# Performance work log

Measured on AMD Instinct MI355X. Metric: run time of the kernel, lower is better.

The kernel has to match this reference:

```python
import jax, jax.numpy as jnp
import numpy as np

B, S, D = 2, 2048, 2048
H = 16
HD = D // H
SCALE = 1.0 / (HD ** 0.5)


def setup_inputs() -> dict:
    key = jax.random.key(0)
    ks = jax.random.split(key, 9)
    std = 0.02
    return {
        "x": jax.random.normal(ks[0], (B, S, D), dtype=jnp.float32),
        "q_w": jax.random.normal(ks[1], (D, D), dtype=jnp.float32) * std,
        "q_b": jax.random.normal(ks[2], (D,), dtype=jnp.float32) * std,
        "k_w": jax.random.normal(ks[3], (D, D), dtype=jnp.float32) * std,
        "k_b": jax.random.normal(ks[4], (D,), dtype=jnp.float32) * std,
        "v_w": jax.random.normal(ks[5], (D, D), dtype=jnp.float32) * std,
        "v_b": jax.random.normal(ks[6], (D,), dtype=jnp.float32) * std,
        "o_w": jax.random.normal(ks[7], (D, D), dtype=jnp.float32) * std,
        "o_b": jax.random.normal(ks[8], (D,), dtype=jnp.float32) * std,
    }


def reference(x, q_w, q_b, k_w, k_b, v_w, v_b, o_w, o_b):
    # torch Linear: y = x @ W.T + b  (weights stored [out, in])
    b, s, _ = x.shape
    dtype = x.dtype
    q = (x @ q_w.T + q_b).reshape(b, s, H, HD).transpose(0, 2, 1, 3)  # [B,H,S,HD]
    k = (x @ k_w.T + k_b).reshape(b, s, H, HD).transpose(0, 2, 1, 3)
    v = (x @ v_w.T + v_b).reshape(b, s, H, HD).transpose(0, 2, 1, 3)
    scores = jnp.einsum("bhqd,bhkd->bhqk", q, k) * SCALE  # [B,H,S,S]
    # causal mask: positions k > q get -inf (via triu(diagonal=1))
    causal = jnp.triu(jnp.ones((s, s), dtype=bool), k=1)
    scores = jnp.where(causal[None, None], -jnp.inf, scores)
    attn = jax.nn.softmax(scores.astype(jnp.float32), axis=-1).astype(dtype)
    out = jnp.einsum("bhqk,bhkd->bhqd", attn, v)  # [B,H,S,HD]
    out = out.transpose(0, 2, 1, 3).reshape(b, s, H * HD)
    return out @ o_w.T + o_b
```

## Files before the change

kernel.cpp:

```cpp
#include <hip/hip_runtime.h>
#include <hip/hip_bf16.h>

#define S_LEN 2048
#define DMODEL 2048
#define NH 16
#define HDIM 128
#define SCALE_F 0.08838834764831845f

typedef __attribute__((ext_vector_type(8))) short bf16x8;
typedef __attribute__((ext_vector_type(4))) float f32x4;

__device__ __forceinline__ unsigned short f2bf(float f) {
  unsigned int u = __float_as_uint(f);
  u += 0x7FFFu + ((u >> 16) & 1u);
  return (unsigned short)(u >> 16);
}

__device__ __forceinline__ void gload16(const void* g, void* l) {
  __builtin_amdgcn_global_load_lds(
      (const __attribute__((address_space(1))) unsigned int*)g,
      (__attribute__((address_space(3))) unsigned int*)l, 16, 0, 0);
}

__global__ __launch_bounds__(256) void cvt_all(
    const float* __restrict__ x, const float* __restrict__ qw,
    const float* __restrict__ kw, const float* __restrict__ vw,
    const float* __restrict__ ow, unsigned short* __restrict__ xb,
    unsigned short* __restrict__ wqkv, unsigned short* __restrict__ wo) {
  int i = blockIdx.x * blockDim.x + threadIdx.x;
  const float* src;
  unsigned short* dst;
  int off;
  if (i < 2097152) {
    src = x; dst = xb; off = i;
  } else {
    const int j = i - 2097152;
    const int wsel = j >> 20;
    off = j & 1048575;
    src = (wsel == 0) ? qw : (wsel == 1) ? kw : (wsel == 2) ? vw : ow;
    dst = (wsel == 0) ? wqkv
        : (wsel == 1) ? (wqkv + 4194304)
        : (wsel == 2) ? (wqkv + 8388608)
                      : wo;
  }
  const float4 v = *(const float4*)(src + (size_t)off * 4);
  ushort4 o;
  o.x = f2bf(v.x); o.y = f2bf(v.y); o.z = f2bf(v.z); o.w = f2bf(v.w);
  *(ushort4*)(dst + (size_t)off * 4) = o;
}

__device__ __forceinline__ void gemm_core_128x256(
    const unsigned short* __restrict__ Ag, const unsigned short* __restrict__ Wg,
    int m0, int n0, char* lds, int t, f32x4 (&acc)[4][4]) {
  const int lane = t & 63, w = t >> 6;
  const int wr = w >> 2, wc = w & 3;

#pragma unroll
  for (int mi = 0; mi < 4; ++mi)
#pragma unroll
    for (int nj = 0; nj < 4; ++nj)
#pragma unroll
      for (int e = 0; e < 4; ++e) acc[mi][nj][e] = 0.f;

  const int fr = lane & 15;
  const int sw16 = (((lane >> 4) ^ ((lane >> 1) & 3)) << 4);
  const int aRowBase = (wr * 64 + fr) * 64;
  const int bRowBase = (wc * 64 + fr) * 64;

  const int cg8 = (((t & 3) ^ ((t >> 3) & 3)) * 8);
  const unsigned short* sAbase = Ag + (m0 + (t >> 2)) * DMODEL + cg8;
  const unsigned short* sBbase0 = Wg + (n0 + (t >> 2)) * DMODEL + cg8;
  const unsigned short* sBbase1 = sBbase0 + 128 * DMODEL;
  char* dstW = lds + w * 1024;

  auto stage3 = [&](int Tc, int h, int buf) {
    const int koff = Tc * 64 + h * 32;
    gload16(sAbase + koff, dstW + buf * 16384 + h * 8192);
    gload16(sBbase0 + koff, dstW + 49152 + buf * 32768 + h * 16384);
    gload16(sBbase1 + koff, dstW + 49152 + buf * 32768 + h * 16384 + 8192);
  };

  auto phase = [&](int h, int bufR, int doStage, int TS, int bufS, int vm) {
    const int rA = bufR * 16384 + h * 8192;
    const int rB = 49152 + bufR * 32768 + h * 16384;
    bf16x8 a[4], b[4];
#pragma unroll
    for (int mi = 0; mi < 4; ++mi)
      a[mi] = *(const bf16x8*)(lds + rA + aRowBase + mi * 1024 + sw16);
#pragma unroll
    for (int nj = 0; nj < 4; ++nj)
      b[nj] = *(const bf16x8*)(lds + rB + bRowBase + nj * 1024 + sw16);
    if (doStage) stage3(TS, h, bufS);
    if (vm == 6) asm volatile("s_waitcnt vmcnt(6)" ::: "memory");
    if (vm == 0) asm volatile("s_waitcnt vmcnt(0)" ::: "memory");
    __builtin_amdgcn_s_barrier();
    __builtin_amdgcn_s_setprio(1);
#pragma unroll
    for (int mi = 0; mi < 4; ++mi)
#pragma unroll
      for (int nj = 0; nj < 4; ++nj)
        acc[mi][nj] = __builtin_amdgcn_mfma_f32_16x16x32_bf16(
            a[mi], b[nj], acc[mi][nj], 0, 0, 0);
    __builtin_amdgcn_s_setprio(0);
    __builtin_amdgcn_s_barrier();
  };

  stage3(0, 0, 0);
  stage3(0, 1, 0);
  stage3(1, 0, 1);
  stage3(1, 1, 1);
  asm volatile("s_waitcnt vmcnt(6)" ::: "memory");
  __builtin_amdgcn_s_barrier();

#pragma unroll 1
  for (int k3 = 0; k3 < 10; ++k3) {
    const int T = k3 * 3;
    phase(0, 0, 1, T + 2, 2, -1);
    phase(1, 0, 1, T + 2, 2, 6);
    phase(0, 1, 1, T + 3, 0, -1);
    phase(1, 1, 1, T + 3, 0, 6);
    phase(0, 2, 1, T + 4, 1, -1);
    phase(1, 2, 1, T + 4, 1, 6);
  }
  phase(0, 0, 0, 0, 0, -1);
  phase(1, 0, 0, 0, 0, 0);
  phase(0, 1, 0, 0, 0, -1);
  phase(1, 1, 0, 0, 0, -1);
}

__global__ __launch_bounds__(512, 1) void gemm_qkv(
    const unsigned short* __restrict__ A, const unsigned short* __restrict__ W,
    const float* __restrict__ qbias, const float* __restrict__ kbias,
    const float* __restrict__ vbias,
    unsigned short* __restrict__ qo, unsigned short* __restrict__ ko,
    unsigned short* __restrict__ vto) {
  extern __shared__ char lds[];
  const int t = threadIdx.x;
  const int swz = ((int)blockIdx.x & 7) * 96 + ((int)blockIdx.x >> 3);
  const int m0 = (swz & 31) * 128;
  const int n0 = (swz >> 5) * 256;

  f32x4 acc[4][4];
  gemm_core_128x256(A, W, m0, n0, lds, t, acc);

  const int lane = t & 63, w = t >> 6;
  const int wr = w >> 2, wc = w & 3;
  const int b_ = m0 >> 11;
  const int proj = n0 >> 11;
  const int nn_base = (n0 & 2047) + wc * 64;
  const float* bias = (proj == 0) ? qbias : ((proj == 1) ? kbias : vbias);
#pragma unroll
  for (int nj = 0; nj < 4; ++nj) {
    const int nn = nn_base + nj * 16 + (lane & 15);
    const int h = nn >> 7, hd = nn & 127;
    const float bv = bias[nn];
#pragma unroll
    for (int mi = 0; mi < 4; ++mi) {
      const int mrow = m0 + wr * 64 + mi * 16 + (lane >> 4) * 4;
      const int s = mrow & 2047;
      if (proj == 2) {
        unsigned short* dst = vto + ((b_ * NH + h) * HDIM + hd) * S_LEN + s;
        ushort4 pk;
        pk.x = f2bf(acc[mi][nj][0] + bv);
        pk.y = f2bf(acc[mi][nj][1] + bv);
        pk.z = f2bf(acc[mi][nj][2] + bv);
        pk.w = f2bf(acc[mi][nj][3] + bv);
        *(ushort4*)dst = pk;
      } else {
        unsigned short* dst =
            ((proj == 0) ? qo : ko) + ((b_ * NH + h) * S_LEN + s) * HDIM + hd;
#pragma unroll
        for (int r = 0; r < 4; r++) dst[r * HDIM] = f2bf(acc[mi][nj][r] + bv);
      }
    }
  }
}

__global__ __launch_bounds__(512, 1) void gemm_out(
    const unsigned short* __restrict__ A, const unsigned short* __restrict__ W,
    const float* __restrict__ bias, float* __restrict__ out) {
  extern __shared__ char lds[];
  const int t = threadIdx.x;
  const int swz = ((int)blockIdx.x & 7) * 32 + ((int)blockIdx.x >> 3);
  const int m0 = (swz & 31) * 128;
  const int n0 = (swz >> 5) * 256;

  f32x4 acc[4][4];
  gemm_core_128x256(A, W, m0, n0, lds, t, acc);

  const int lane = t & 63, w = t >> 6;
  const int wr = w >> 2, wc = w & 3;
#pragma unroll
  for (int nj = 0; nj < 4; ++nj) {
    const int n = n0 + wc * 64 + nj * 16 + (lane & 15);
    const float bv = bias[n];
#pragma unroll
    for (int mi = 0; mi < 4; ++mi) {
      const int mrow = m0 + wr * 64 + mi * 16 + (lane >> 4) * 4;
      float* dst = out + (size_t)mrow * DMODEL + n;
#pragma unroll
      for (int r = 0; r < 4; r++) dst[r * DMODEL] = acc[mi][nj][r] + bv;
    }
  }
}

__global__ __launch_bounds__(256, 2) void attn_fwd(
    const unsigned short* __restrict__ Q,
    const unsigned short* __restrict__ K,
    const unsigned short* __restrict__ VT,
    unsigned short* __restrict__ ctx) {
  __shared__ unsigned short Ks[2][64 * 128];
  __shared__ unsigned short Vs[2][128 * 64];
  __shared__ unsigned short Ps[4][16 * 64];
  const int t = threadIdx.x, lane = t & 63, w = t >> 6;
  const int bh = blockIdx.y;
  const unsigned short* Qb = Q + bh * (S_LEN * HDIM);
  const unsigned short* Kb = K + bh * (S_LEN * HDIM);
  const unsigned short* Vb = VT + bh * (HDIM * S_LEN);
  const int b_ = bh >> 4, h = bh & 15;

  auto stageKV = [&](int buf, int kv0) {
#pragma unroll
    for (int u = 0; u < 4; ++u) {
      const int c = t + u * 256;
      const int row = c >> 4, cc = c & 15;
      gload16(Kb + (kv0 + row) * HDIM + ((cc ^ (row & 7)) * 8),
              (char*)Ks[buf] + u * 4096 + w * 1024);
    }
#pragma unroll
    for (int u = 0; u < 4; ++u) {
      const int c = t + u * 256;
      const int row = c >> 3, cc = c & 7;
      gload16(Vb + row * S_LEN + kv0 + ((cc ^ (row & 7)) * 8),
              (char*)Vs[buf] + u * 4096 + w * 1024);
    }
  };

#pragma unroll 1
  for (int pi = 0; pi < 2; ++pi) {
    const int qtile = pi ? (31 - blockIdx.x) : blockIdx.x;
    const int q0 = qtile * 64 + w * 16;

    bf16x8 qf[4];
    {
      const unsigned short* qrow =
          Qb + (q0 + (lane & 15)) * HDIM + (lane >> 4) * 8;
#pragma unroll
      for (int dk = 0; dk < 4; dk++) qf[dk] = *(const bf16x8*)(qrow + dk * 32);
    }

    float mrow[4], lrow[4];
    f32x4 oacc[8];
#pragma unroll
    for (int r = 0; r < 4; r++) { mrow[r] = -__builtin_inff(); lrow[r] = 0.f; }
#pragma unroll
    for (int d = 0; d < 8; d++)
#pragma unroll
      for (int e = 0; e < 4; e++) oacc[d][e] = 0.f;

    const int nt = qtile + 1;
    stageKV(0, 0);
    __syncthreads();
    int cur = 0;

#pragma unroll 1
    for (int kt = 0; kt < nt; ++kt) {
      if (kt + 1 < nt) stageKV(cur ^ 1, (kt + 1) * 64);

      const unsigned short* Kc = Ks[cur];
      const unsigned short* Vc = Vs[cur];
      const int kv0 = kt * 64;

      f32x4 sacc[4];
#pragma unroll
      for (int ck = 0; ck < 4; ck++)
#pragma unroll
        for (int e = 0; e < 4; e++) sacc[ck][e] = 0.f;
      __builtin_amdgcn_s_setprio(1);
#pragma unroll
      for (int ck = 0; ck < 4; ++ck) {
        const int krow = ck * 16 + (lane & 15);
#pragma unroll
        for (int dk = 0; dk < 4; ++dk) {
          const int chunk = dk * 4 + (lane >> 4);
          const bf16x8 kf = *(const bf16x8*)((const char*)Kc + krow * 256 +
                                             ((chunk ^ (krow & 7)) << 4));
          sacc[ck] = __builtin_amdgcn_mfma_f32_16x16x32_bf16(qf[dk], kf,
                                                             sacc[ck], 0, 0, 0);
        }
      }
      __builtin_amdgcn_s_setprio(0);
#pragma unroll
      for (int ck = 0; ck < 4; ck++)
#pragma unroll
        for (int r = 0; r < 4; r++) sacc[ck][r] *= SCALE_F;
      if (kt == qtile) {
#pragma unroll
        for (int ck = 0; ck < 4; ck++) {
          const int col = kv0 + ck * 16 + (lane & 15);
#pragma unroll
          for (int r = 0; r < 4; r++) {
            const int rowq = q0 + (lane >> 4) * 4 + r;
            if (col > rowq) sacc[ck][r] = -__builtin_inff();
          }
        }
      }
      float tmax[4];
#pragma unroll
      for (int r = 0; r < 4; r++)
        tmax[r] = fmaxf(fmaxf(sacc[0][r], sacc[1][r]),
                        fmaxf(sacc[2][r], sacc[3][r]));
#pragma unroll
      for (int off = 1; off < 16; off <<= 1)
#pragma unroll
        for (int r = 0; r < 4; r++)
          tmax[r] = fmaxf(tmax[r], __shfl_xor(tmax[r], off, 64));
      bool need = false;
#pragma unroll
      for (int r = 0; r < 4; r++) need |= (tmax[r] > mrow[r] + 8.f);
      if (__any(need)) {
#pragma unroll
        for (int r = 0; r < 4; r++) {
          const float mn = fmaxf(mrow[r], tmax[r]);
          const float corr = __expf(mrow[r] - mn);
          mrow[r] = mn;
          lrow[r] *= corr;
#pragma unroll
          for (int d = 0; d < 8; d++) oacc[d][r] *= corr;
        }
      }
      float rsum[4] = {0.f, 0.f, 0.f, 0.f};
#pragma unroll
      for (int ck = 0; ck < 4; ck++)
#pragma unroll
        for (int r = 0; r < 4; r++) {
          const float p = __expf(sacc[ck][r] - mrow[r]);
          rsum[r] += p;
          const int prow = (lane >> 4) * 4 + r;
          const int pcol = ck * 16 + (lane & 15);
          *(unsigned short*)((char*)Ps[w] +
                             ((prow * 128 + pcol * 2) ^ ((prow & 7) << 4))) =
              f2bf(p);
        }
#pragma unroll
      for (int off = 1; off < 16; off <<= 1)
#pragma unroll
        for (int r = 0; r < 4; r++) rsum[r] += __shfl_xor(rsum[r], off, 64);
#pragma unroll
      for (int r = 0; r < 4; r++) lrow[r] += rsum[r];

      bf16x8 pf[2];
      {
        const int prow = lane & 15;
#pragma unroll
        for (int kk = 0; kk < 2; kk++) {
          const int chunk = kk * 4 + (lane >> 4);
          pf[kk] = *(const bf16x8*)((const char*)Ps[w] + prow * 128 +
                                    ((chunk ^ (prow & 7)) << 4));
        }
      }
      __builtin_amdgcn_s_setprio(1);
#pragma unroll
      for (int d = 0; d < 8; ++d) {
        const int vrow = d * 16 + (lane & 15);
#pragma unroll
        for (int kk = 0; kk < 2; ++kk) {
          const int chunk = kk * 4 + (lane >> 4);
          const bf16x8 vf = *(const bf16x8*)((const char*)Vc + vrow * 128 +
                                             ((chunk ^ (vrow & 7)) << 4));
          oacc[d] = __builtin_amdgcn_mfma_f32_16x16x32_bf16(pf[kk], vf, oacc[d],
                                                            0, 0, 0);
        }
      }
      __builtin_amdgcn_s_setprio(0);

      __syncthreads();
      cur ^= 1;
    }

#pragma unroll
    for (int r = 0; r < 4; r++) {
      const float inv = 1.f / lrow[r];
      const int srow = q0 + (lane >> 4) * 4 + r;
      unsigned short* dst =
          ctx + (b_ * S_LEN + srow) * DMODEL + h * HDIM + (lane & 15);
#pragma unroll
      for (int d = 0; d < 8; d++) dst[d * 16] = f2bf(oacc[d][r] * inv);
    }
  }
}

extern "C" void kernel_launch(void* const* d_in, const int* in_sizes, int n_in,
                              void* d_out, int out_size, void* d_ws,
                              size_t ws_size, hipStream_t stream) {
  const float* x  = (const float*)d_in[0];
  const float* qw = (const float*)d_in[1];
  const float* qb = (const float*)d_in[2];
  const float* kw = (const float*)d_in[3];
  const float* kb = (const float*)d_in[4];
  const float* vw = (const float*)d_in[5];
  const float* vb = (const float*)d_in[6];
  const float* ow = (const float*)d_in[7];
  const float* ob = (const float*)d_in[8];
  float* out = (float*)d_out;

  unsigned short* xb   = (unsigned short*)d_ws;
  unsigned short* wqkv = xb + (size_t)8388608;
  unsigned short* wo   = wqkv + (size_t)12582912;
  unsigned short* qt_  = wo + (size_t)4194304;
  unsigned short* kt_  = qt_ + (size_t)8388608;
  unsigned short* vt_  = kt_ + (size_t)8388608;
  unsigned short* ctx  = vt_ + (size_t)8388608;

  cvt_all<<<24576, 256, 0, stream>>>(x, qw, kw, vw, ow, xb, wqkv, wo);

  gemm_qkv<<<768, 512, 147456, stream>>>(xb, wqkv, qb, kb, vb, qt_, kt_, vt_);
  attn_fwd<<<dim3(16, 32), 256, 0, stream>>>(qt_, kt_, vt_, ctx);
  gemm_out<<<256, 512, 147456, stream>>>(ctx, wo, ob, out);
}
```

Measured before the change: 279.9 us.

## Use 256x256 tiles with double-buffered phased pipeline for QKV GEMM

Replaces the 128x256 QKV projection GEMM core with a new 256x256 tile core. Each tile is split into four phases that interleave LDS fragment reads, async global-to-LDS staging of the next K tile into a double buffer, and MFMA work under setprio. This halves the grid to 384 blocks and raises arithmetic intensity per block, cutting global traffic for A and W. The cost is more accumulator registers per thread and fewer blocks, so load balance and wave quantization across CUs change.

Result: no change. 274.9 us (-1.8%).

```diff
diff --git a/kernel.cpp b/kernel.cpp
--- a/kernel.cpp
+++ b/kernel.cpp
@@ -49,6 +49,181 @@
   *(ushort4*)(dst + (size_t)off * 4) = o;
 }
 
+#define VMW(n) asm volatile("s_waitcnt vmcnt(" #n ")" ::: "memory")
+
+#define STAGE_A(Tn, mh, buf)                                                  \
+  do {                                                                        \
+    gload16(sA + (size_t)((mh)*64 + w * 8) * DMODEL + (Tn)*64,                \
+            lds + (buf)*32768 + ((mh)*64 + w * 8) * 128);                     \
+    gload16(sA + (size_t)((mh)*64 + 128 + w * 8) * DMODEL + (Tn)*64,          \
+            lds + (buf)*32768 + ((mh)*64 + 128 + w * 8) * 128);               \
+  } while (0)
+
+#define STAGE_B(Tn, nh, buf)                                                  \
+  do {                                                                        \
+    const int p0_ = (w & 3) * 8 + (w >> 2) * 64 + (nh)*32;                    \
+    gload16(sB + (size_t)(p0_)*DMODEL + (Tn)*64,                              \
+            lds + 65536 + (buf)*32768 + (p0_)*128);                           \
+    gload16(sB + (size_t)(p0_ + 128) * DMODEL + (Tn)*64,                      \
+            lds + 65536 + (buf)*32768 + (p0_ + 128) * 128);                   \
+  } while (0)
+
+#define LDA(mh, buf)                                                          \
+  do {                                                                        \
+    _Pragma("unroll") for (int mi2 = 0; mi2 < 4; ++mi2) {                     \
+      a[mi2][0] = *(const bf16x8*)(lds + (buf)*32768 + aBase +                \
+                                   ((mh)*4 + mi2) * 2048 + sks0);             \
+      a[mi2][1] = *(const bf16x8*)(lds + (buf)*32768 + aBase +                \
+                                   ((mh)*4 + mi2) * 2048 + sks1);             \
+    }                                                                         \
+  } while (0)
+
+#define LDB(nh, buf)                                                          \
+  do {                                                                        \
+    _Pragma("unroll") for (int nj2 = 0; nj2 < 2; ++nj2) {                     \
+      b[nh][nj2][0] = *(const bf16x8*)(lds + (buf)*32768 + bBase +            \
+                                       ((nh)*2 + nj2) * 2048 + sks0);         \
+      b[nh][nj2][1] = *(const bf16x8*)(lds + (buf)*32768 + bBase +            \
+                                       ((nh)*2 + nj2) * 2048 + sks1);         \
+    }                                                                         \
+  } while (0)
+
+#define MM(mh, nh)                                                            \
+  do {                                                                        \
+    _Pragma("unroll") for (int mi2 = 0; mi2 < 4; ++mi2)                       \
+        _Pragma("unroll") for (int nj2 = 0; nj2 < 2; ++nj2) {                 \
+      acc[(mh)*4 + mi2][(nh)*2 + nj2] =                                       \
+          __builtin_amdgcn_mfma_f32_16x16x32_bf16(                            \
+              a[mi2][0], b[nh][nj2][0], acc[(mh)*4 + mi2][(nh)*2 + nj2], 0,   \
+              0, 0);                                                          \
+      acc[(mh)*4 + mi2][(nh)*2 + nj2] =                                       \
+          __builtin_amdgcn_mfma_f32_16x16x32_bf16(                            \
+              a[mi2][1], b[nh][nj2][1], acc[(mh)*4 + mi2][(nh)*2 + nj2], 0,   \
+              0, 0);                                                          \
+    }                                                                         \
+  } while (0)
+
+#define PHASE(RD, ST, VM, MH, NH)                                             \
+  do {                                                                        \
+    RD;                                                                       \
+    ST;                                                                       \
+    VM;                                                                       \
+    __builtin_amdgcn_s_barrier();                                             \
+    asm volatile("s_waitcnt lgkmcnt(0)" ::: "memory");                        \
+    __builtin_amdgcn_s_setprio(1);                                            \
+    MM(MH, NH);                                                               \
+    __builtin_amdgcn_s_setprio(0);                                            \
+    __builtin_amdgcn_s_barrier();                                             \
+  } while (0)
+
+#define TILE_STD(buf, Tn)                                                     \
+  do {                                                                        \
+    PHASE(LDA(0, buf); LDB(0, buf),                                           \
+          STAGE_A(Tn, 0, (buf) ^ 1); STAGE_B(Tn, 0, (buf) ^ 1), VMW(6), 0, 0);\
+    PHASE(LDB(1, buf), STAGE_B(Tn, 1, (buf) ^ 1), VMW(6), 0, 1);              \
+    PHASE(LDA(1, buf), STAGE_A(Tn, 1, (buf) ^ 1), , 1, 1);                    \
+    PHASE(, , VMW(4), 1, 0);                                                  \
+  } while (0)
+
+#define TILE_LAST(buf)                                                        \
+  do {                                                                        \
+    PHASE(LDA(0, buf); LDB(0, buf), , VMW(2), 0, 0);                          \
+    PHASE(LDB(1, buf), , VMW(0), 0, 1);                                       \
+    PHASE(LDA(1, buf), , , 1, 1);                                             \
+    PHASE(, , , 1, 0);                                                        \
+  } while (0)
+
+__device__ __forceinline__ void gemm_core_256(
+    const unsigned short* __restrict__ Ag, const unsigned short* __restrict__ Wg,
+    int m0, int n0, char* lds, int t, f32x4 (&acc)[8][4]) {
+  const int lane = t & 63, w = t >> 6;
+  const int wr = w >> 2, wc = w & 3;
+
+#pragma unroll
+  for (int mi = 0; mi < 8; ++mi)
+#pragma unroll
+    for (int nj = 0; nj < 4; ++nj)
+#pragma unroll
+      for (int e = 0; e < 4; ++e) acc[mi][nj][e] = 0.f;
+
+  const int fr = lane & 15;
+  const int sks0 = (((lane >> 4) ^ (lane & 7)) << 4);
+  const int sks1 = sks0 ^ 64;
+  const int aBase = (wr * 128 + fr) * 128;
+  const int bBase = 65536 + (wc * 64 + fr) * 128;
+
+  const int srow = lane >> 3;
+  const int schunk = ((lane & 7) ^ (lane >> 3)) * 8;
+  const unsigned short* sA = Ag + (size_t)(m0 + srow) * DMODEL + schunk;
+  const unsigned short* sB = Wg + (size_t)(n0 + srow) * DMODEL + schunk;
+
+  bf16x8 a[4][2];
+  bf16x8 b[2][2][2];
+
+  STAGE_A(0, 0, 0);
+  STAGE_A(0, 1, 0);
+  STAGE_B(0, 0, 0);
+  STAGE_B(0, 1, 0);
+  VMW(0);
+  __builtin_amdgcn_s_barrier();
+
+#pragma unroll 1
+  for (int T = 0; T < 30; T += 2) {
+    TILE_STD(0, T + 1);
+    TILE_STD(1, T + 2);
+  }
+  TILE_STD(0, 31);
+  TILE_LAST(1);
+}
+
+__global__ __launch_bounds__(512, 1) void gemm_qkv(
+    const unsigned short* __restrict__ A, const unsigned short* __restrict__ W,
+    const float* __restrict__ qbias, const float* __restrict__ kbias,
+    const float* __restrict__ vbias,
+    unsigned short* __restrict__ qo, unsigned short* __restrict__ ko,
+    unsigned short* __restrict__ vto) {
+  extern __shared__ char lds[];
+  const int t = threadIdx.x;
+  const int swz = ((int)blockIdx.x & 7) * 48 + ((int)blockIdx.x >> 3);
+  const int m0 = (swz & 15) * 256;
+  const int n0 = (swz >> 4) * 256;
+
+  f32x4 acc[8][4];
+  gemm_core_256(A, W, m0, n0, lds, t, acc);
+
+  const int lane = t & 63, w = t >> 6;
+  const int wr = w >> 2, wc = w & 3;
+  const int b_ = m0 >> 11;
+  const int proj = n0 >> 11;
+  const int nn_base = (n0 & 2047) + wc * 64;
+  const float* bias = (proj == 0) ? qbias : ((proj == 1) ? kbias : vbias);
+#pragma unroll
+  for (int nj = 0; nj < 4; ++nj) {
+    const int nn = nn_base + nj * 16 + (lane & 15);
+    const int h = nn >> 7, hd = nn & 127;
+    const float bv = bias[nn];
+#pragma unroll
+    for (int mi = 0; mi < 8; ++mi) {
+      const int mrow = m0 + wr * 128 + mi * 16 + (lane >> 4) * 4;
+      const int s = mrow & 2047;
+      if (proj == 2) {
+        unsigned short* dst = vto + ((b_ * NH + h) * HDIM + hd) * S_LEN + s;
+        ushort4 pk;
+        pk.x = f2bf(acc[mi][nj][0] + bv);
+        pk.y = f2bf(acc[mi][nj][1] + bv);
+        pk.z = f2bf(acc[mi][nj][2] + bv);
+        pk.w = f2bf(acc[mi][nj][3] + bv);
+        *(ushort4*)dst = pk;
+      } else {
+        unsigned short* dst =
+            ((proj == 0) ? qo : ko) + ((b_ * NH + h) * S_LEN + s) * HDIM + hd;
+#pragma unroll
+        for (int r = 0; r < 4; r++) dst[r * HDIM] = f2bf(acc[mi][nj][r] + bv);
+      }
+    }
+  }
+}
+
 __device__ __forceinline__ void gemm_core_128x256(
     const unsigned short* __restrict__ Ag, const unsigned short* __restrict__ Wg,
     int m0, int n0, char* lds, int t, f32x4 (&acc)[4][4]) {
@@ -128,54 +303,6 @@
   phase(1, 1, 0, 0, 0, -1);
 }
 
-__global__ __launch_bounds__(512, 1) void gemm_qkv(
-    const unsigned short* __restrict__ A, const unsigned short* __restrict__ W,
-    const float* __restrict__ qbias, const float* __restrict__ kbias,
-    const float* __restrict__ vbias,
-    unsigned short* __restrict__ qo, unsigned short* __restrict__ ko,
-    unsigned short* __restrict__ vto) {
-  extern __shared__ char lds[];
-  const int t = threadIdx.x;
-  const int swz = ((int)blockIdx.x & 7) * 96 + ((int)blockIdx.x >> 3);
-  const int m0 = (swz & 31) * 128;
-  const int n0 = (swz >> 5) * 256;
-
-  f32x4 acc[4][4];
-  gemm_core_128x256(A, W, m0, n0, lds, t, acc);
-
-  const int lane = t & 63, w = t >> 6;
-  const int wr = w >> 2, wc = w & 3;
-  const int b_ = m0 >> 11;
-  const int proj = n0 >> 11;
-  const int nn_base = (n0 & 2047) + wc * 64;
-  const float* bias = (proj == 0) ? qbias : ((proj == 1) ? kbias : vbias);
-#pragma unroll
-  for (int nj = 0; nj < 4; ++nj) {
-    const int nn = nn_base + nj * 16 + (lane & 15);
-    const int h = nn >> 7, hd = nn & 127;
-    const float bv = bias[nn];
-#pragma unroll
-    for (int mi = 0; mi < 4; ++mi) {
-      const int mrow = m0 + wr * 64 + mi * 16 + (lane >> 4) * 4;
-      const int s = mrow & 2047;
-      if (proj == 2) {
-        unsigned short* dst = vto + ((b_ * NH + h) * HDIM + hd) * S_LEN + s;
-        ushort4 pk;
-        pk.x = f2bf(acc[mi][nj][0] + bv);
-        pk.y = f2bf(acc[mi][nj][1] + bv);
-        pk.z = f2bf(acc[mi][nj][2] + bv);
-        pk.w = f2bf(acc[mi][nj][3] + bv);
-        *(ushort4*)dst = pk;
-      } else {
-        unsigned short* dst =
-            ((proj == 0) ? qo : ko) + ((b_ * NH + h) * S_LEN + s) * HDIM + hd;
-#pragma unroll
-        for (int r = 0; r < 4; r++) dst[r * HDIM] = f2bf(acc[mi][nj][r] + bv);
-      }
-    }
-  }
-}
-
 __global__ __launch_bounds__(512, 1) void gemm_out(
     const unsigned short* __restrict__ A, const unsigned short* __restrict__ W,
     const float* __restrict__ bias, float* __restrict__ out) {
@@ -414,7 +541,7 @@
 
   cvt_all<<<24576, 256, 0, stream>>>(x, qw, kw, vw, ow, xb, wqkv, wo);
 
-  gemm_qkv<<<768, 512, 147456, stream>>>(xb, wqkv, qb, kb, vb, qt_, kt_, vt_);
+  gemm_qkv<<<384, 512, 131072, stream>>>(xb, wqkv, qb, kb, vb, qt_, kt_, vt_);
   attn_fwd<<<dim3(16, 32), 256, 0, stream>>>(qt_, kt_, vt_, ctx);
   gemm_out<<<256, 512, 147456, stream>>>(ctx, wo, ob, out);
 }
```

## Stage QKV epilogue through LDS for coalesced stores, defer row-sum reduction, remap attention grid

Applied to the files above, without the earlier changes.

The QKV GEMM epilogue now writes bias-added bf16 tiles into LDS, then stores them with 16-byte vector writes, in the transposed layout for V and the head-major layout for Q and K. This replaces scattered 2-byte and 8-byte global stores. The attention kernel keeps per-lane partial row sums and does the cross-lane shuffle reduction once at the end instead of on every KV tile. It also switches to a 1D grid whose mapping spreads heads across blocks. The risks are an extra barrier and LDS reuse after the GEMM main loop, which must be safe, and a different rounding order in the row sum.

Result: faster. 266.5 us (-4.8%).

```diff
diff --git a/kernel.cpp b/kernel.cpp
--- a/kernel.cpp
+++ b/kernel.cpp
@@ -149,29 +149,61 @@
   const int proj = n0 >> 11;
   const int nn_base = (n0 & 2047) + wc * 64;
   const float* bias = (proj == 0) ? qbias : ((proj == 1) ? kbias : vbias);
-#pragma unroll
-  for (int nj = 0; nj < 4; ++nj) {
-    const int nn = nn_base + nj * 16 + (lane & 15);
-    const int h = nn >> 7, hd = nn & 127;
-    const float bv = bias[nn];
-#pragma unroll
-    for (int mi = 0; mi < 4; ++mi) {
-      const int mrow = m0 + wr * 64 + mi * 16 + (lane >> 4) * 4;
-      const int s = mrow & 2047;
-      if (proj == 2) {
-        unsigned short* dst = vto + ((b_ * NH + h) * HDIM + hd) * S_LEN + s;
+
+  if (proj == 2) {
+    unsigned short* Tv = (unsigned short*)lds;
+#pragma unroll
+    for (int nj = 0; nj < 4; ++nj) {
+      const int col = wc * 64 + nj * 16 + (lane & 15);
+      const float bv = bias[nn_base - wc * 64 + col - (nj * 16 + (lane & 15)) +
+                            nj * 16 + (lane & 15)];
+#pragma unroll
+      for (int mi = 0; mi < 4; ++mi) {
+        const int row0 = wr * 64 + mi * 16 + (lane >> 4) * 4;
         ushort4 pk;
         pk.x = f2bf(acc[mi][nj][0] + bv);
         pk.y = f2bf(acc[mi][nj][1] + bv);
         pk.z = f2bf(acc[mi][nj][2] + bv);
         pk.w = f2bf(acc[mi][nj][3] + bv);
-        *(ushort4*)dst = pk;
-      } else {
-        unsigned short* dst =
-            ((proj == 0) ? qo : ko) + ((b_ * NH + h) * S_LEN + s) * HDIM + hd;
-#pragma unroll
-        for (int r = 0; r < 4; r++) dst[r * HDIM] = f2bf(acc[mi][nj][r] + bv);
-      }
+        *(ushort4*)&Tv[col * 136 + row0] = pk;
+      }
+    }
+    __syncthreads();
+    const int col = t >> 1, half = t & 1;
+    const int nn = (n0 & 2047) + col;
+    const int h = nn >> 7, hd = nn & 127;
+    unsigned short* base =
+        vto + (size_t)((b_ * NH + h) * HDIM + hd) * S_LEN + (m0 & 2047) +
+        half * 64;
+#pragma unroll
+    for (int u = 0; u < 8; ++u)
+      *(bf16x8*)(base + u * 8) =
+          *(const bf16x8*)&Tv[col * 136 + half * 64 + u * 8];
+  } else {
+    unsigned short* Tq = (unsigned short*)lds;
+#pragma unroll
+    for (int nj = 0; nj < 4; ++nj) {
+      const int col = wc * 64 + nj * 16 + (lane & 15);
+      const float bv = bias[(n0 & 2047) + col];
+#pragma unroll
+      for (int mi = 0; mi < 4; ++mi) {
+        const int row0 = wr * 64 + mi * 16 + (lane >> 4) * 4;
+#pragma unroll
+        for (int r = 0; r < 4; ++r)
+          Tq[(row0 + r) * 264 + col] = f2bf(acc[mi][nj][r] + bv);
+      }
+    }
+    __syncthreads();
+    const int lr = t >> 2, qc = t & 3;
+    const int s = (m0 & 2047) + lr;
+    unsigned short* qk = (proj == 0) ? qo : ko;
+#pragma unroll
+    for (int u = 0; u < 8; ++u) {
+      const int lc = qc * 64 + u * 8;
+      const int nn = (n0 & 2047) + lc;
+      const int h = nn >> 7, hd = nn & 127;
+      *(bf16x8*)(qk + (size_t)((b_ * NH + h) * S_LEN + s) * HDIM + hd) =
+          *(const bf16x8*)&Tq[lr * 264 + lc];
     }
   }
 }
@@ -213,7 +245,9 @@
   __shared__ unsigned short Vs[2][128 * 64];
   __shared__ unsigned short Ps[4][16 * 64];
   const int t = threadIdx.x, lane = t & 63, w = t >> 6;
-  const int bh = blockIdx.y;
+  const int bid = blockIdx.x;
+  const int bh = ((bid & 7) << 2) + ((bid >> 3) & 3);
+  const int xq = bid >> 5;
   const unsigned short* Qb = Q + bh * (S_LEN * HDIM);
   const unsigned short* Kb = K + bh * (S_LEN * HDIM);
   const unsigned short* Vb = VT + bh * (HDIM * S_LEN);
@@ -238,7 +272,7 @@
 
 #pragma unroll 1
   for (int pi = 0; pi < 2; ++pi) {
-    const int qtile = pi ? (31 - blockIdx.x) : blockIdx.x;
+    const int qtile = pi ? (31 - xq) : xq;
     const int q0 = qtile * 64 + w * 16;
 
     bf16x8 qf[4];
@@ -329,25 +363,18 @@
           for (int d = 0; d < 8; d++) oacc[d][r] *= corr;
         }
       }
-      float rsum[4] = {0.f, 0.f, 0.f, 0.f};
 #pragma unroll
       for (int ck = 0; ck < 4; ck++)
 #pragma unroll
         for (int r = 0; r < 4; r++) {
           const float p = __expf(sacc[ck][r] - mrow[r]);
-          rsum[r] += p;
+          lrow[r] += p;
           const int prow = (lane >> 4) * 4 + r;
           const int pcol = ck * 16 + (lane & 15);
           *(unsigned short*)((char*)Ps[w] +
                              ((prow * 128 + pcol * 2) ^ ((prow & 7) << 4))) =
               f2bf(p);
         }
-#pragma unroll
-      for (int off = 1; off < 16; off <<= 1)
-#pragma unroll
-        for (int r = 0; r < 4; r++) rsum[r] += __shfl_xor(rsum[r], off, 64);
-#pragma unroll
-      for (int r = 0; r < 4; r++) lrow[r] += rsum[r];
 
       bf16x8 pf[2];
       {
@@ -378,6 +405,10 @@
       cur ^= 1;
     }
 
+#pragma unroll
+    for (int off = 1; off < 16; off <<= 1)
+#pragma unroll
+      for (int r = 0; r < 4; r++) lrow[r] += __shfl_xor(lrow[r], off, 64);
 #pragma unroll
     for (int r = 0; r < 4; r++) {
       const float inv = 1.f / lrow[r];
@@ -415,6 +446,6 @@
   cvt_all<<<24576, 256, 0, stream>>>(x, qw, kw, vw, ow, xb, wqkv, wo);
 
   gemm_qkv<<<768, 512, 147456, stream>>>(xb, wqkv, qb, kb, vb, qt_, kt_, vt_);
-  attn_fwd<<<dim3(16, 32), 256, 0, stream>>>(qt_, kt_, vt_, ctx);
+  attn_fwd<<<512, 256, 0, stream>>>(qt_, kt_, vt_, ctx);
   gemm_out<<<256, 512, 147456, stream>>>(ctx, wo, ob, out);
 }
```
